# Performance work log

Measured on AMD Instinct MI355X. Metric: run time of the kernel, lower is better.

The kernel has to match this reference:

```python
import jax, jax.numpy as jnp
import numpy as np

EMBED_DIM = 768
NUM_HEADS = 12
HEAD_DIM = EMBED_DIM // NUM_HEADS


def setup_inputs() -> dict:
    key = jax.random.key(0)
    k_x, k_wqkv, k_bqkv, k_wp, k_bp = jax.random.split(key, 5)
    B, S, D = 4, 2048, EMBED_DIM
    # nn.Linear default init scale ~ 1/sqrt(fan_in); exact distribution irrelevant for a reference
    lim = 1.0 / np.sqrt(D)
    x = jax.random.normal(k_x, (B, S, D), dtype=jnp.float32)
    w_qkv = jax.random.uniform(k_wqkv, (D, 3 * D), jnp.float32, -lim, lim)
    b_qkv = jax.random.uniform(k_bqkv, (3 * D,), jnp.float32, -lim, lim)
    w_proj = jax.random.uniform(k_wp, (D, D), jnp.float32, -lim, lim)
    b_proj = jax.random.uniform(k_bp, (D,), jnp.float32, -lim, lim)
    return {"x": x, "w_qkv": w_qkv, "b_qkv": b_qkv, "w_proj": w_proj, "b_proj": b_proj}


def reference(x, w_qkv, b_qkv, w_proj, b_proj):
    B, S, D = x.shape
    H, Hd = NUM_HEADS, HEAD_DIM
    qkv = x @ w_qkv + b_qkv                      # [B,S,3D]
    qkv = qkv.reshape(B, S, 3, H, Hd)
    qkv = jnp.transpose(qkv, (2, 0, 3, 1, 4))     # [3,B,H,S,Hd]
    q, k, v = qkv[0], qkv[1], qkv[2]
    scale = 1.0 / np.sqrt(Hd).astype(np.float32)
    scores = jnp.einsum("bhsd,bhtd->bhst", q, k) * scale  # [B,H,S,S]
    attn = jax.nn.softmax(scores, axis=-1)
    out = jnp.einsum("bhst,bhtd->bhsd", attn, v)  # [B,H,S,Hd]
    out = jnp.transpose(out, (0, 2, 1, 3)).reshape(B, S, D)
    return out @ w_proj + b_proj
```

## Files before the change

kernel.cpp:

```cpp
#include <hip/hip_runtime.h>


typedef _Float16 f16;
typedef _Float16 f16x8 __attribute__((ext_vector_type(8)));
typedef _Float16 f16x4 __attribute__((ext_vector_type(4)));
typedef float f32x4 __attribute__((ext_vector_type(4)));

#define BQ 4
#define SQ 2048
#define DQ 768
#define HQ 12
#define HD 64
#define M_TOK (BQ*SQ)
#define KVB 64
#define NT (SQ/KVB)
#define QSCALE 0.18033688f
#define THR_LOG2 11.5f

__device__ __forceinline__ void gld_lds16(const f16* g, f16* l) {
  __builtin_amdgcn_global_load_lds((const __attribute__((address_space(1))) void*)g,
                                   (__attribute__((address_space(3))) void*)l,
                                   16, 0, 0);
}

__global__ __launch_bounds__(256)
void prep(const float* __restrict__ x, f16* __restrict__ xh,
          const float* __restrict__ w_qkv, f16* __restrict__ wqkvT,
          const float* __restrict__ w_proj, f16* __restrict__ wprojT)
{
  __shared__ float tile[32][33];
  const int bid = blockIdx.x, tid = threadIdx.x;
  if (bid < 6144) {
    int i = (bid * 256 + tid) * 4;
    float4 v = *(const float4*)(x + i);
    f16x4 o = { (f16)v.x, (f16)v.y, (f16)v.z, (f16)v.w };
    *(f16x4*)(xh + i) = o;
    return;
  }
  const float* w; f16* wt; int K, N, nb, kb;
  if (bid < 7872) {
    int b2 = bid - 6144; w = w_qkv; wt = wqkvT; K = DQ; N = 3 * DQ;
    nb = (b2 % 72) * 32; kb = (b2 / 72) * 32;
  } else {
    int b3 = bid - 7872; w = w_proj; wt = wprojT; K = DQ; N = DQ;
    nb = (b3 % 24) * 32; kb = (b3 / 24) * 32;
  }
  int tx = tid & 31, ty = tid >> 5;
  for (int r = ty; r < 32; r += 8)
    tile[r][tx] = w[(size_t)(kb + r) * N + nb + tx];
  __syncthreads();
  for (int r = ty; r < 32; r += 8)
    wt[(size_t)(nb + r) * K + kb + tx] = (f16)tile[tx][r];
}

template<int MODE>
__global__ __launch_bounds__(256, 2)
void gemm128(const f16* __restrict__ A, const f16* __restrict__ Bt,
             const float* __restrict__ bias, float* __restrict__ Cf,
             f16* __restrict__ Qb, f16* __restrict__ Kb, f16* __restrict__ Vt,
             int M, int N, int K, int nbx)
{
  __shared__ f16 Ash[2][128 * 32];
  __shared__ f16 Bsh[2][128 * 32];
  const int tid = threadIdx.x;
  const int bid = blockIdx.x;
  const int nb = bid % nbx, mb = bid / nbx;
  const int m0 = mb * 128, n0 = nb * 128;
  const int lane = tid & 63, wid = tid >> 6;
  const int wr = wid >> 1, wc = wid & 1;
  const int l16 = lane & 15, l4 = lane >> 4;

  f32x4 acc[4][4] = {};

  const int f0 = tid, f1 = tid + 256;
  const f16* a0 = A + (size_t)(m0 + (f0 >> 2)) * K + (f0 & 3) * 8;
  const f16* a1 = A + (size_t)(m0 + (f1 >> 2)) * K + (f1 & 3) * 8;
  const f16* b0 = Bt + (size_t)(n0 + (f0 >> 2)) * K + (f0 & 3) * 8;
  const f16* b1 = Bt + (size_t)(n0 + (f1 >> 2)) * K + (f1 & 3) * 8;

#define GSTAGE(buf, k0)                                   \
  do {                                                    \
    gld_lds16(a0 + (k0), Ash[buf] + f0 * 8);              \
    gld_lds16(a1 + (k0), Ash[buf] + f1 * 8);              \
    gld_lds16(b0 + (k0), Bsh[buf] + f0 * 8);              \
    gld_lds16(b1 + (k0), Bsh[buf] + f1 * 8);              \
  } while (0)

  GSTAGE(0, 0);
  __syncthreads();
  for (int k0 = 0; k0 < K; k0 += 32) {
    const int buf = (k0 >> 5) & 1;
    if (k0 + 32 < K) GSTAGE(buf ^ 1, k0 + 32);
    f16x8 af[4], bfr[4];
    #pragma unroll
    for (int m = 0; m < 4; ++m)
      af[m] = *(const f16x8*)(Ash[buf] + (wr * 64 + m * 16 + l16) * 32 + l4 * 8);
    #pragma unroll
    for (int n = 0; n < 4; ++n)
      bfr[n] = *(const f16x8*)(Bsh[buf] + (wc * 64 + n * 16 + l16) * 32 + l4 * 8);
    #pragma unroll
    for (int m = 0; m < 4; ++m)
      #pragma unroll
      for (int n = 0; n < 4; ++n)
        acc[m][n] = __builtin_amdgcn_mfma_f32_16x16x32_f16(af[m], bfr[n], acc[m][n], 0, 0, 0);
    __syncthreads();
  }
#undef GSTAGE

  const int cbase = n0 + wc * 64;
  const int rbase = m0 + wr * 64;
  if (MODE == 1) {
    #pragma unroll
    for (int n = 0; n < 4; ++n) {
      int c = cbase + n * 16 + l16;
      float bv = bias[c];
      #pragma unroll
      for (int m = 0; m < 4; ++m)
        #pragma unroll
        for (int r = 0; r < 4; ++r) {
          int rr = rbase + m * 16 + l4 * 4 + r;
          Cf[(size_t)rr * N + c] = acc[m][n][r] + bv;
        }
    }
  } else {
    #pragma unroll
    for (int n = 0; n < 4; ++n) {
      int c = cbase + n * 16 + l16;
      float bv = bias[c];
      int which = c / DQ;
      int rem = c - which * DQ;
      int h = rem >> 6, hd = rem & 63;
      #pragma unroll
      for (int m = 0; m < 4; ++m) {
        int rr0 = rbase + m * 16 + l4 * 4;
        int b = rr0 >> 11, s = rr0 & 2047;
        size_t bh = (size_t)(b * HQ + h);
        if (which == 2) {
          f16x4 ov = { (f16)(acc[m][n][0] + bv), (f16)(acc[m][n][1] + bv),
                       (f16)(acc[m][n][2] + bv), (f16)(acc[m][n][3] + bv) };
          *(f16x4*)(Vt + (bh * HD + hd) * SQ + s) = ov;
        } else if (which == 0) {
          #pragma unroll
          for (int r = 0; r < 4; ++r)
            Qb[(bh * SQ + s + r) * HD + hd] = (f16)((acc[m][n][r] + bv) * QSCALE);
        } else {
          #pragma unroll
          for (int r = 0; r < 4; ++r)
            Kb[(bh * SQ + s + r) * HD + hd] = (f16)(acc[m][n][r] + bv);
        }
      }
    }
  }
}

__device__ __forceinline__ int permK(int p) {
  return ((p & 16) << 1) | (((p >> 2) & 3) << 3) | ((p & 32) >> 3) | (p & 3);
}

__global__ __launch_bounds__(256, 3)
void attn(const f16* __restrict__ Qb, const f16* __restrict__ Kb,
          const f16* __restrict__ Vt, f16* __restrict__ O)
{
  __shared__ f16 Ksh[2][KVB * HD];
  __shared__ f16 Vsh[2][HD * KVB];
  const int tid = threadIdx.x, lane = tid & 63, wid = tid >> 6;
  const int l16 = lane & 15, l4 = lane >> 4;

  const int nwg = gridDim.x;
  const int cpx = nwg >> 3;
  const int swz = (blockIdx.x & 7) * cpx + (blockIdx.x >> 3);
  const int qt = swz & 15, bh = swz >> 4;
  const int b = bh / HQ, h = bh - b * HQ;
  const f16* q  = Qb + (size_t)bh * SQ * HD;
  const f16* kp = Kb + (size_t)bh * SQ * HD;
  const f16* vp = Vt + (size_t)bh * HD * SQ;
  const int s0 = qt * 128 + wid * 32;

  f16x8 qf[2][2];
  #pragma unroll
  for (int g = 0; g < 2; ++g)
    #pragma unroll
    for (int kk = 0; kk < 2; ++kk)
      qf[g][kk] = *(const f16x8*)(q + (size_t)(s0 + g * 16 + l16) * HD + kk * 32 + l4 * 8);

  f32x4 oacc[2][4] = {};
  float mrun[2] = { -1e30f, -1e30f }, lrun[2] = { 0.f, 0.f };

  const int p0 = tid >> 3, p1 = (tid >> 3) + 32;
  const int scS = ((tid & 7) ^ (p0 & 7)) * 8;
  const int kr0 = permK(p0), kr1 = permK(p1);

#define STAGE_K(buf, toff)                                                     \
  do {                                                                         \
    gld_lds16(kp + (size_t)((toff) + kr0) * HD + scS, Ksh[buf] + tid * 8);     \
    gld_lds16(kp + (size_t)((toff) + kr1) * HD + scS, Ksh[buf] + (tid + 256) * 8);\
  } while (0)
#define STAGE_V(buf, toff)                                                     \
  do {                                                                         \
    gld_lds16(vp + (size_t)p0 * SQ + (toff) + scS, Vsh[buf] + tid * 8);        \
    gld_lds16(vp + (size_t)p1 * SQ + (toff) + scS, Vsh[buf] + (tid + 256) * 8);\
  } while (0)

  auto QKT = [&](f32x4 (&S)[2][4], int kbuf) {
    #pragma unroll
    for (int g = 0; g < 2; ++g)
      #pragma unroll
      for (int n = 0; n < 4; ++n)
        S[g][n] = (f32x4){0.f, 0.f, 0.f, 0.f};
    const f16* Kbase = Ksh[kbuf];
    __builtin_amdgcn_s_setprio(1);
    #pragma unroll
    for (int kk = 0; kk < 2; ++kk) {
      f16x8 kf[4];
      #pragma unroll
      for (int n = 0; n < 4; ++n)
        kf[n] = *(const f16x8*)(Kbase + (n * 16 + l16) * HD +
                                ((kk * 32 + l4 * 8) ^ ((l16 & 7) * 8)));
      #pragma unroll
      for (int n = 0; n < 4; ++n) {
        S[0][n] = __builtin_amdgcn_mfma_f32_16x16x32_f16(kf[n], qf[0][kk], S[0][n], 0, 0, 0);
        S[1][n] = __builtin_amdgcn_mfma_f32_16x16x32_f16(kf[n], qf[1][kk], S[1][n], 0, 0, 0);
      }
    }
    __builtin_amdgcn_s_setprio(0);
  };

  auto SMPV = [&](f32x4 (&S)[2][4], int vbuf) {
    f16x8 bfr[2][2];
    #pragma unroll
    for (int g = 0; g < 2; ++g) {
      float rm = -1e30f;
      #pragma unroll
      for (int n = 0; n < 4; ++n)
        rm = fmaxf(rm, fmaxf(fmaxf(S[g][n][0], S[g][n][1]),
                             fmaxf(S[g][n][2], S[g][n][3])));
      rm = fmaxf(rm, __shfl_xor(rm, 16));
      rm = fmaxf(rm, __shfl_xor(rm, 32));
      if (!__all(rm - mrun[g] <= THR_LOG2)) {
        float mn = fmaxf(mrun[g], rm);
        float corr = __builtin_amdgcn_exp2f(mrun[g] - mn);
        lrun[g] *= corr;
        #pragma unroll
        for (int n = 0; n < 4; ++n)
          oacc[g][n] *= corr;
        mrun[g] = mn;
      }
      float mref = mrun[g];
      float ps = 0.f;
      #pragma unroll
      for (int n = 0; n < 4; ++n)
        #pragma unroll
        for (int r = 0; r < 4; ++r) {
          float pv = __builtin_amdgcn_exp2f(S[g][n][r] - mref);
          bfr[g][n & 1][(n >> 1) * 4 + r] = (f16)pv;
          ps += pv;
        }
      ps += __shfl_xor(ps, 16);
      ps += __shfl_xor(ps, 32);
      lrun[g] += ps;
    }
    const f16* Vbase = Vsh[vbuf];
    __builtin_amdgcn_s_setprio(1);
    #pragma unroll
    for (int kk = 0; kk < 2; ++kk) {
      f16x8 vf[4];
      #pragma unroll
      for (int n = 0; n < 4; ++n)
        vf[n] = *(const f16x8*)(Vbase + (n * 16 + l16) * KVB +
                                ((kk * 32 + l4 * 8) ^ ((l16 & 7) * 8)));
      #pragma unroll
      for (int n = 0; n < 4; ++n) {
        oacc[0][n] = __builtin_amdgcn_mfma_f32_16x16x32_f16(vf[n], bfr[0][kk], oacc[0][n], 0, 0, 0);
        oacc[1][n] = __builtin_amdgcn_mfma_f32_16x16x32_f16(vf[n], bfr[1][kk], oacc[1][n], 0, 0, 0);
      }
    }
    __builtin_amdgcn_s_setprio(0);
  };

  f32x4 sA[2][4], sB[2][4];

  STAGE_K(0, 0);
  __syncthreads();
  STAGE_K(1, KVB);
  STAGE_V(0, 0);
  QKT(sA, 0);
  __syncthreads();

  for (int t = 1; t < NT; t += 2) {
    if (t + 1 < NT) STAGE_K((t + 1) & 1, (t + 1) * KVB);
    STAGE_V(t & 1, t * KVB);
    QKT(sB, t & 1);
    SMPV(sA, (t - 1) & 1);
    __syncthreads();
    if (t + 1 < NT) {
      if (t + 2 < NT) STAGE_K((t + 2) & 1, (t + 2) * KVB);
      STAGE_V((t + 1) & 1, (t + 1) * KVB);
      QKT(sA, (t + 1) & 1);
      SMPV(sB, t & 1);
      __syncthreads();
    }
  }
  SMPV(sB, (NT - 1) & 1);

#undef STAGE_K
#undef STAGE_V

  #pragma unroll
  for (int g = 0; g < 2; ++g) {
    float inv = 1.f / lrun[g];
    const int s = s0 + g * 16 + l16;
    f16* obase = O + ((size_t)b * SQ + s) * DQ + h * HD + l4 * 4;
    #pragma unroll
    for (int n = 0; n < 4; ++n) {
      f16x4 ov = { (f16)(oacc[g][n][0] * inv), (f16)(oacc[g][n][1] * inv),
                   (f16)(oacc[g][n][2] * inv), (f16)(oacc[g][n][3] * inv) };
      *(f16x4*)(obase + n * 16) = ov;
    }
  }
}

extern "C" void kernel_launch(void* const* d_in, const int* in_sizes, int n_in,
                              void* d_out, int out_size, void* d_ws, size_t ws_size,
                              hipStream_t stream) {
  const float* x      = (const float*)d_in[0];
  const float* w_qkv  = (const float*)d_in[1];
  const float* b_qkv  = (const float*)d_in[2];
  const float* w_proj = (const float*)d_in[3];
  const float* b_proj = (const float*)d_in[4];
  float* out = (float*)d_out;

  char* ws = (char*)d_ws;
  f16* xh     = (f16*)ws; ws += (size_t)M_TOK * DQ * 2;
  f16* wqkvT  = (f16*)ws; ws += (size_t)3 * DQ * DQ * 2;
  f16* wprojT = (f16*)ws; ws += (size_t)DQ * DQ * 2;
  f16* Qb     = (f16*)ws; ws += (size_t)M_TOK * DQ * 2;
  f16* Kb     = (f16*)ws; ws += (size_t)M_TOK * DQ * 2;
  f16* Vt     = (f16*)ws; ws += (size_t)M_TOK * DQ * 2;
  f16* AO     = xh;

  prep<<<8448, 256, 0, stream>>>(x, xh, w_qkv, wqkvT, w_proj, wprojT);

  gemm128<0><<<(M_TOK / 128) * (3 * DQ / 128), 256, 0, stream>>>(
      xh, wqkvT, b_qkv, nullptr, Qb, Kb, Vt, M_TOK, 3 * DQ, DQ, 3 * DQ / 128);

  attn<<<BQ * HQ * (SQ / 128), 256, 0, stream>>>(Qb, Kb, Vt, AO);

  gemm128<1><<<(M_TOK / 128) * (DQ / 128), 256, 0, stream>>>(
      AO, wprojT, b_proj, out, nullptr, nullptr, nullptr, M_TOK, DQ, DQ, DQ / 128);
}
```

Before: 165.8 us.

## Load K/V fragments straight from global into registers, drop LDS staging

The attention kernel no longer stages K and V tiles through double-buffered shared memory with async global-to-LDS copies and block barriers. Each wave now loads its own K and V MFMA fragments directly from global memory into registers, prefetching the next K tile during softmax, and the QK/softmax software pipeline is simplified to one tile per iteration. This removes barriers and LDS traffic, but each of the four waves now reads the same K/V data separately. That means roughly four times the global/L2 traffic and less latency hiding.

```diff
diff --git a/kernel.cpp b/kernel.cpp
--- a/kernel.cpp
+++ b/kernel.cpp
@@ -161,8 +161,6 @@
 void attn(const f16* __restrict__ Qb, const f16* __restrict__ Kb,
           const f16* __restrict__ Vt, f16* __restrict__ O)
 {
-  __shared__ f16 Ksh[2][KVB * HD];
-  __shared__ f16 Vsh[2][HD * KVB];
   const int tid = threadIdx.x, lane = tid & 63, wid = tid >> 6;
   const int l16 = lane & 15, l4 = lane >> 4;
 
@@ -186,54 +184,55 @@
   f32x4 oacc[2][4] = {};
   float mrun[2] = { -1e30f, -1e30f }, lrun[2] = { 0.f, 0.f };
 
-  const int p0 = tid >> 3, p1 = (tid >> 3) + 32;
-  const int scS = ((tid & 7) ^ (p0 & 7)) * 8;
-  const int kr0 = permK(p0), kr1 = permK(p1);
-
-#define STAGE_K(buf, toff)                                                     \
-  do {                                                                         \
-    gld_lds16(kp + (size_t)((toff) + kr0) * HD + scS, Ksh[buf] + tid * 8);     \
-    gld_lds16(kp + (size_t)((toff) + kr1) * HD + scS, Ksh[buf] + (tid + 256) * 8);\
+  const f16* kpl[4];
+  const f16* vpl[4];
+  #pragma unroll
+  for (int n = 0; n < 4; ++n) {
+    kpl[n] = kp + (size_t)permK(n * 16 + l16) * HD + l4 * 8;
+    vpl[n] = vp + (size_t)(n * 16 + l16) * SQ + l4 * 8;
+  }
+
+  f16x8 kf[2][4], vf[2][4];
+
+#define LOADK(t0)                                                             \
+  do {                                                                        \
+    _Pragma("unroll")                                                         \
+    for (int kk = 0; kk < 2; ++kk)                                            \
+      _Pragma("unroll")                                                       \
+      for (int n = 0; n < 4; ++n)                                             \
+        kf[kk][n] = *(const f16x8*)(kpl[n] + (size_t)(t0) * HD + kk * 32);    \
   } while (0)
-#define STAGE_V(buf, toff)                                                     \
-  do {                                                                         \
-    gld_lds16(vp + (size_t)p0 * SQ + (toff) + scS, Vsh[buf] + tid * 8);        \
-    gld_lds16(vp + (size_t)p1 * SQ + (toff) + scS, Vsh[buf] + (tid + 256) * 8);\
+#define LOADV(t0)                                                             \
+  do {                                                                        \
+    _Pragma("unroll")                                                         \
+    for (int kk = 0; kk < 2; ++kk)                                            \
+      _Pragma("unroll")                                                       \
+      for (int n = 0; n < 4; ++n)                                             \
+        vf[kk][n] = *(const f16x8*)(vpl[n] + (t0) + kk * 32);                 \
   } while (0)
 
-  auto QKT = [&](f32x4 (&S)[2][4], int kbuf) {
-    #pragma unroll
-    for (int g = 0; g < 2; ++g)
-      #pragma unroll
-      for (int n = 0; n < 4; ++n)
-        S[g][n] = (f32x4){0.f, 0.f, 0.f, 0.f};
-    const f16* Kbase = Ksh[kbuf];
+  LOADK(0);
+  for (int t = 0; t < NT; ++t) {
+    LOADV(t * KVB);
+    f32x4 sacc[2][4] = {};
     __builtin_amdgcn_s_setprio(1);
     #pragma unroll
-    for (int kk = 0; kk < 2; ++kk) {
-      f16x8 kf[4];
-      #pragma unroll
-      for (int n = 0; n < 4; ++n)
-        kf[n] = *(const f16x8*)(Kbase + (n * 16 + l16) * HD +
-                                ((kk * 32 + l4 * 8) ^ ((l16 & 7) * 8)));
+    for (int kk = 0; kk < 2; ++kk)
       #pragma unroll
       for (int n = 0; n < 4; ++n) {
-        S[0][n] = __builtin_amdgcn_mfma_f32_16x16x32_f16(kf[n], qf[0][kk], S[0][n], 0, 0, 0);
-        S[1][n] = __builtin_amdgcn_mfma_f32_16x16x32_f16(kf[n], qf[1][kk], S[1][n], 0, 0, 0);
+        sacc[0][n] = __builtin_amdgcn_mfma_f32_16x16x32_f16(kf[kk][n], qf[0][kk], sacc[0][n], 0, 0, 0);
+        sacc[1][n] = __builtin_amdgcn_mfma_f32_16x16x32_f16(kf[kk][n], qf[1][kk], sacc[1][n], 0, 0, 0);
       }
-    }
     __builtin_amdgcn_s_setprio(0);
-  };
-
-  auto SMPV = [&](f32x4 (&S)[2][4], int vbuf) {
+    if (t + 1 < NT) LOADK((t + 1) * KVB);
     f16x8 bfr[2][2];
     #pragma unroll
     for (int g = 0; g < 2; ++g) {
       float rm = -1e30f;
       #pragma unroll
       for (int n = 0; n < 4; ++n)
-        rm = fmaxf(rm, fmaxf(fmaxf(S[g][n][0], S[g][n][1]),
-                             fmaxf(S[g][n][2], S[g][n][3])));
+        rm = fmaxf(rm, fmaxf(fmaxf(sacc[g][n][0], sacc[g][n][1]),
+                             fmaxf(sacc[g][n][2], sacc[g][n][3])));
       rm = fmaxf(rm, __shfl_xor(rm, 16));
       rm = fmaxf(rm, __shfl_xor(rm, 32));
       if (!__all(rm - mrun[g] <= THR_LOG2)) {
@@ -251,7 +250,7 @@
       for (int n = 0; n < 4; ++n)
         #pragma unroll
         for (int r = 0; r < 4; ++r) {
-          float pv = __builtin_amdgcn_exp2f(S[g][n][r] - mref);
+          float pv = __builtin_amdgcn_exp2f(sacc[g][n][r] - mref);
           bfr[g][n & 1][(n >> 1) * 4 + r] = (f16)pv;
           ps += pv;
         }
@@ -259,51 +258,18 @@
       ps += __shfl_xor(ps, 32);
       lrun[g] += ps;
     }
-    const f16* Vbase = Vsh[vbuf];
     __builtin_amdgcn_s_setprio(1);
     #pragma unroll
-    for (int kk = 0; kk < 2; ++kk) {
-      f16x8 vf[4];
-      #pragma unroll
-      for (int n = 0; n < 4; ++n)
-        vf[n] = *(const f16x8*)(Vbase + (n * 16 + l16) * KVB +
-                                ((kk * 32 + l4 * 8) ^ ((l16 & 7) * 8)));
+    for (int kk = 0; kk < 2; ++kk)
       #pragma unroll
       for (int n = 0; n < 4; ++n) {
-        oacc[0][n] = __builtin_amdgcn_mfma_f32_16x16x32_f16(vf[n], bfr[0][kk], oacc[0][n], 0, 0, 0);
-        oacc[1][n] = __builtin_amdgcn_mfma_f32_16x16x32_f16(vf[n], bfr[1][kk], oacc[1][n], 0, 0, 0);
+        oacc[0][n] = __builtin_amdgcn_mfma_f32_16x16x32_f16(vf[kk][n], bfr[0][kk], oacc[0][n], 0, 0, 0);
+        oacc[1][n] = __builtin_amdgcn_mfma_f32_16x16x32_f16(vf[kk][n], bfr[1][kk], oacc[1][n], 0, 0, 0);
       }
-    }
     __builtin_amdgcn_s_setprio(0);
-  };
-
-  f32x4 sA[2][4], sB[2][4];
-
-  STAGE_K(0, 0);
-  __syncthreads();
-  STAGE_K(1, KVB);
-  STAGE_V(0, 0);
-  QKT(sA, 0);
-  __syncthreads();
-
-  for (int t = 1; t < NT; t += 2) {
-    if (t + 1 < NT) STAGE_K((t + 1) & 1, (t + 1) * KVB);
-    STAGE_V(t & 1, t * KVB);
-    QKT(sB, t & 1);
-    SMPV(sA, (t - 1) & 1);
-    __syncthreads();
-    if (t + 1 < NT) {
-      if (t + 2 < NT) STAGE_K((t + 2) & 1, (t + 2) * KVB);
-      STAGE_V((t + 1) & 1, (t + 1) * KVB);
-      QKT(sA, (t + 1) & 1);
-      SMPV(sB, t & 1);
-      __syncthreads();
-    }
-  }
-  SMPV(sB, (NT - 1) & 1);
-
-#undef STAGE_K
-#undef STAGE_V
+  }
+#undef LOADK
+#undef LOADV
 
   #pragma unroll
   for (int g = 0; g < 2; ++g) {
```

After: 262.5 us. 1.58x slower.
